# Performance work log

Measured on AMD Instinct MI355X. Metric: run time of the kernel, lower is better.

Reference implementation:

```python
import jax, jax.numpy as jnp
import numpy as np

N_NODES = 100000
N_EDGES = 1600000
IN_FEATS = 128
HIDDEN = 256
NUM_CLASSES = 1


def setup_inputs() -> dict:
    key = jax.random.key(0)
    ks = jax.random.split(key, 6)
    x = jax.random.normal(ks[0], (N_NODES, IN_FEATS), dtype=jnp.float32)
    src = jax.random.randint(ks[1], (N_EDGES,), 0, N_NODES, dtype=jnp.int64 if jax.config.jax_enable_x64 else jnp.int32).astype(jnp.int32)
    dst = jax.random.randint(ks[2], (N_EDGES,), 0, N_NODES, dtype=jnp.int32)
    W1 = jax.random.normal(ks[3], (IN_FEATS, HIDDEN), dtype=jnp.float32) * (1.0 / np.sqrt(IN_FEATS))
    b1 = jnp.zeros((HIDDEN,), dtype=jnp.float32)
    W2 = jax.random.normal(ks[4], (HIDDEN, NUM_CLASSES), dtype=jnp.float32) * (1.0 / np.sqrt(HIDDEN))
    b2 = jnp.zeros((NUM_CLASSES,), dtype=jnp.float32)
    return {"x": x, "src": src, "dst": dst, "W1": W1, "b1": b1, "W2": W2, "b2": b2}


def _graph_conv(x, src, dst, W, b):
    """DGL GraphConv with norm='both': D_out^{-1/2} gather -> scatter-add -> D_in^{-1/2}, then XW+b."""
    n = x.shape[0]
    ones = jnp.ones(src.shape[0], dtype=x.dtype)
    deg_out = jax.ops.segment_sum(ones, src, num_segments=n)
    deg_in = jax.ops.segment_sum(ones, dst, num_segments=n)
    norm_out = jax.lax.rsqrt(jnp.maximum(deg_out, 1.0))  # [N]
    norm_in = jax.lax.rsqrt(jnp.maximum(deg_in, 1.0))    # [N]
    h = x * norm_out[:, None]                 # [N, F]
    msg = h[src]                              # [E, F] gather (memory-bound)
    agg = jax.ops.segment_sum(msg, dst, num_segments=n)  # [N, F] scatter-add
    agg = agg * norm_in[:, None]
    return agg @ W + b


def reference(x, src, dst, W1, b1, W2, b2):
    # layer 0: GraphConv -> relu (dropout p=0.0 -> identity)
    h = jax.nn.relu(_graph_conv(x, src, dst, W1, b1))
    # output layer: GraphConv -> sigmoid
    h = jax.nn.sigmoid(_graph_conv(h, src, dst, W2, b2))
    return h
```

## Files before the change

kernel.cpp:

```cpp
#include <hip/hip_runtime.h>
#include <math.h>

#define NN 100000
#define NE 1600000
#define INF 128
#define HID 256
#define SCAN_BLK 256
#define NSCAN ((NN + SCAN_BLK - 1) / SCAN_BLK)
#define FGRP 8
#define FRNG (NN / FGRP)
#define NC 32
#define CHUNK (NE / NC)

typedef short bf16x8 __attribute__((ext_vector_type(8)));
typedef float f32x4 __attribute__((ext_vector_type(4)));

__device__ __forceinline__ unsigned int f2bf(float f) {
    unsigned int u = __float_as_uint(f);
    u = u + 0x7FFFu + ((u >> 16) & 1u);
    return u >> 16;
}

__launch_bounds__(1024)
__global__ void k_hist(const int* __restrict__ src, const int* __restrict__ dst,
                       int* __restrict__ hist_out, int* __restrict__ hist_in) {
    __shared__ int h[FRNG];
    const int type = blockIdx.x & 1;
    const int g = (blockIdx.x >> 1) & (FGRP - 1);
    const int c = blockIdx.x >> 4;
    const int lo = g * FRNG;
    for (int i = threadIdx.x; i < FRNG; i += 1024) h[i] = 0;
    __syncthreads();
    const int4* a4 = reinterpret_cast<const int4*>((type ? dst : src) + c * CHUNK);
    for (int k = threadIdx.x; k < CHUNK / 4; k += 1024) {
        int4 v = a4[k];
        int i0 = v.x - lo, i1 = v.y - lo, i2 = v.z - lo, i3 = v.w - lo;
        if ((unsigned)i0 < FRNG) atomicAdd(&h[i0], 1);
        if ((unsigned)i1 < FRNG) atomicAdd(&h[i1], 1);
        if ((unsigned)i2 < FRNG) atomicAdd(&h[i2], 1);
        if ((unsigned)i3 < FRNG) atomicAdd(&h[i3], 1);
    }
    __syncthreads();
    int* out = (type ? hist_in : hist_out) + (size_t)c * NN + lo;
    for (int i = threadIdx.x; i < FRNG; i += 1024) out[i] = h[i];
}

__global__ void k_norms2(const int* __restrict__ hist_out, const int* __restrict__ hist_in,
                         float* __restrict__ nrm_out, float* __restrict__ nrm_in,
                         int* __restrict__ deg_in) {
    int v = blockIdx.x * blockDim.x + threadIdx.x;
    if (v < NN) {
        int so = 0, si = 0;
        #pragma unroll
        for (int b = 0; b < NC; ++b) {
            so += hist_out[(size_t)b * NN + v];
            si += hist_in[(size_t)b * NN + v];
        }
        nrm_out[v] = rsqrtf(fmaxf((float)so, 1.0f));
        nrm_in[v]  = rsqrtf(fmaxf((float)si, 1.0f));
        deg_in[v]  = si;
    }
}

__global__ void k_xconv(const float* __restrict__ x, const float* __restrict__ nrm_out,
                        unsigned int* __restrict__ xs) {
    int i = blockIdx.x * blockDim.x + threadIdx.x;
    if (i >= NN * (INF / 2)) return;
    int row = i >> 6;
    float n = nrm_out[row];
    float2 v = *reinterpret_cast<const float2*>(x + (size_t)i * 2);
    xs[i] = f2bf(v.x * n) | (f2bf(v.y * n) << 16);
}

__global__ void k_wfrag(const float* __restrict__ W1, const float* __restrict__ b1,
                        const float* __restrict__ W2, unsigned short* __restrict__ fragW,
                        float2* __restrict__ bw) {
    int idx = blockIdx.x * blockDim.x + threadIdx.x;
    if (idx < 4096) {
        int l = idx & 63, ks = (idx >> 6) & 3, nt = idx >> 8;
        int kbase = ks * 32 + ((l >> 4) << 3);
        int col = nt * 16 + (l & 15);
        bf16x8 r;
        #pragma unroll
        for (int i = 0; i < 8; ++i)
            r[i] = (short)f2bf(W1[(size_t)(kbase + i) * HID + col]);
        *reinterpret_cast<bf16x8*>(fragW + (size_t)idx * 8) = r;
    } else if (idx < 4096 + HID) {
        int n = idx - 4096;
        bw[n] = make_float2(b1[n], W2[n]);
    }
}

__global__ void k_scan1(const int* __restrict__ deg_in, int* __restrict__ partial) {
    __shared__ int sh[SCAN_BLK];
    int i = blockIdx.x * SCAN_BLK + threadIdx.x;
    int v = (i < NN) ? deg_in[i] : 0;
    sh[threadIdx.x] = v;
    __syncthreads();
    for (int off = SCAN_BLK / 2; off > 0; off >>= 1) {
        if (threadIdx.x < off) sh[threadIdx.x] += sh[threadIdx.x + off];
        __syncthreads();
    }
    if (threadIdx.x == 0) partial[blockIdx.x] = sh[0];
}

__global__ void k_scan2(int* __restrict__ partial) {
    int lane = threadIdx.x;
    int carry = 0;
    for (int c = 0; c < NSCAN; c += 64) {
        int idx = c + lane;
        int v = (idx < NSCAN) ? partial[idx] : 0;
        int s = v;
        #pragma unroll
        for (int off = 1; off < 64; off <<= 1) {
            int t = __shfl_up(s, off, 64);
            if (lane >= off) s += t;
        }
        if (idx < NSCAN) partial[idx] = s - v + carry;
        carry += __shfl(s, 63, 64);
    }
}

__global__ void k_scan3(const int* __restrict__ deg_in, const int* __restrict__ partial,
                        int* __restrict__ offsets) {
    __shared__ int sh[SCAN_BLK];
    int i = blockIdx.x * SCAN_BLK + threadIdx.x;
    int v = (i < NN) ? deg_in[i] : 0;
    sh[threadIdx.x] = v;
    __syncthreads();
    for (int off = 1; off < SCAN_BLK; off <<= 1) {
        int t = (threadIdx.x >= off) ? sh[threadIdx.x - off] : 0;
        __syncthreads();
        sh[threadIdx.x] += t;
        __syncthreads();
    }
    int ex = sh[threadIdx.x] - v + partial[blockIdx.x];
    if (i < NN) offsets[i] = ex;
    if (i == 0) offsets[NN] = NE;
}

__global__ void k_cbase(const int* __restrict__ offsets, const int* __restrict__ hist_in,
                        int* __restrict__ cbase) {
    int v = blockIdx.x * blockDim.x + threadIdx.x;
    if (v < NN) {
        int run = offsets[v];
        #pragma unroll
        for (int b = 0; b < NC; ++b) {
            cbase[(size_t)b * NN + v] = run;
            run += hist_in[(size_t)b * NN + v];
        }
    }
}

__launch_bounds__(1024)
__global__ void k_fill2(const int* __restrict__ src, const int* __restrict__ dst,
                        const int* __restrict__ cbase, int* __restrict__ csr_src) {
    __shared__ int cur[FRNG];
    const int g = blockIdx.x & (FGRP - 1);
    const int c = blockIdx.x >> 3;
    const int lo = g * FRNG;
    const int* cb = cbase + (size_t)c * NN + lo;
    for (int i = threadIdx.x; i < FRNG; i += 1024) cur[i] = cb[i];
    __syncthreads();
    const int e0 = c * CHUNK;
    const int4* d4 = reinterpret_cast<const int4*>(dst + e0);
    for (int k = threadIdx.x; k < CHUNK / 4; k += 1024) {
        int4 v = d4[k];
        int e = e0 + k * 4;
        int i0 = v.x - lo, i1 = v.y - lo, i2 = v.z - lo, i3 = v.w - lo;
        if ((unsigned)i0 < FRNG) { int p = atomicAdd(&cur[i0], 1); csr_src[p] = src[e]; }
        if ((unsigned)i1 < FRNG) { int p = atomicAdd(&cur[i1], 1); csr_src[p] = src[e + 1]; }
        if ((unsigned)i2 < FRNG) { int p = atomicAdd(&cur[i2], 1); csr_src[p] = src[e + 2]; }
        if ((unsigned)i3 < FRNG) { int p = atomicAdd(&cur[i3], 1); csr_src[p] = src[e + 3]; }
    }
}

__global__ void k_gather(const unsigned int* __restrict__ xs, const int* __restrict__ offsets,
                         const int* __restrict__ csr_src, const float* __restrict__ nrm_in,
                         unsigned int* __restrict__ aggb) {
    int row = blockIdx.x * 4 + (threadIdx.x >> 6);
    if (row >= NN) return;
    int lane = threadIdx.x & 63;
    int beg = offsets[row], end = offsets[row + 1];
    float a0 = 0.f, a1 = 0.f, b0 = 0.f, b1 = 0.f;
    float c0 = 0.f, c1 = 0.f, d0 = 0.f, d1 = 0.f;
    int j = beg;
    if (j + 4 <= end) {
        int s0 = csr_src[j], s1 = csr_src[j + 1], s2 = csr_src[j + 2], s3 = csr_src[j + 3];
        while (true) {
            unsigned int p0 = xs[(size_t)s0 * 64 + lane];
            unsigned int p1 = xs[(size_t)s1 * 64 + lane];
            unsigned int p2 = xs[(size_t)s2 * 64 + lane];
            unsigned int p3 = xs[(size_t)s3 * 64 + lane];
            j += 4;
            bool more = (j + 4 <= end);
            if (more) {
                s0 = csr_src[j]; s1 = csr_src[j + 1]; s2 = csr_src[j + 2]; s3 = csr_src[j + 3];
            }
            a0 += __uint_as_float(p0 << 16); a1 += __uint_as_float(p0 & 0xFFFF0000u);
            b0 += __uint_as_float(p1 << 16); b1 += __uint_as_float(p1 & 0xFFFF0000u);
            c0 += __uint_as_float(p2 << 16); c1 += __uint_as_float(p2 & 0xFFFF0000u);
            d0 += __uint_as_float(p3 << 16); d1 += __uint_as_float(p3 & 0xFFFF0000u);
            if (!more) break;
        }
    }
    for (; j < end; ++j) {
        unsigned int p0 = xs[(size_t)csr_src[j] * 64 + lane];
        a0 += __uint_as_float(p0 << 16);
        a1 += __uint_as_float(p0 & 0xFFFF0000u);
    }
    float ni = nrm_in[row];
    float lo = ((a0 + b0) + (c0 + d0)) * ni;
    float hi = ((a1 + b1) + (c1 + d1)) * ni;
    aggb[(size_t)row * 64 + lane] = f2bf(lo) | (f2bf(hi) << 16);
}

__launch_bounds__(256)
__global__ void k_gemm(const unsigned short* __restrict__ aggb,
                       const unsigned short* __restrict__ fragW,
                       const float2* __restrict__ bw, const float* __restrict__ nrm_out,
                       float* __restrict__ z) {
    const int l = threadIdx.x & 63;
    const int w = threadIdx.x >> 6;
    const int r0 = blockIdx.x * 64 + w * 16;
    const int n15 = l & 15;
    const int hi = l >> 4;
    const int arow = r0 + n15;

    bf16x8 a[4];
    if (arow < NN) {
        #pragma unroll
        for (int ks = 0; ks < 4; ++ks)
            a[ks] = *reinterpret_cast<const bf16x8*>(aggb + (size_t)arow * INF + ks * 32 + (hi << 3));
    } else {
        #pragma unroll
        for (int ks = 0; ks < 4; ++ks) a[ks] = (bf16x8){0, 0, 0, 0, 0, 0, 0, 0};
    }

    float pacc[4] = {0.f, 0.f, 0.f, 0.f};
    #pragma unroll
    for (int nt = 0; nt < 16; ++nt) {
        f32x4 acc = {0.f, 0.f, 0.f, 0.f};
        #pragma unroll
        for (int ks = 0; ks < 4; ++ks) {
            bf16x8 b = *reinterpret_cast<const bf16x8*>(fragW + (size_t)(((nt * 4 + ks) * 64 + l) << 3));
            acc = __builtin_amdgcn_mfma_f32_16x16x32_bf16(a[ks], b, acc, 0, 0, 0);
        }
        float2 c = bw[nt * 16 + n15];
        #pragma unroll
        for (int g = 0; g < 4; ++g)
            pacc[g] += fmaxf(acc[g] + c.x, 0.f) * c.y;
    }
    #pragma unroll
    for (int off = 1; off < 16; off <<= 1) {
        #pragma unroll
        for (int g = 0; g < 4; ++g) pacc[g] += __shfl_xor(pacc[g], off, 64);
    }
    if (n15 == 0) {
        #pragma unroll
        for (int g = 0; g < 4; ++g) {
            int gr = r0 + (hi << 2) + g;
            if (gr < NN) z[gr] = nrm_out[gr] * pacc[g];
        }
    }
}

__global__ void k_out(const float* __restrict__ z, const int* __restrict__ offsets,
                      const int* __restrict__ csr_src, const float* __restrict__ nrm_in,
                      const float* __restrict__ b2, float* __restrict__ out) {
    int v = blockIdx.x * 16 + (threadIdx.x >> 4);
    if (v >= NN) return;
    int li = threadIdx.x & 15;
    int beg = offsets[v], end = offsets[v + 1];
    float s = 0.f;
    for (int j = beg + li; j < end; j += 16) s += z[csr_src[j]];
    #pragma unroll
    for (int off = 1; off < 16; off <<= 1) s += __shfl_xor(s, off, 64);
    if (li == 0) {
        float val = s * nrm_in[v] + b2[0];
        out[v] = 1.0f / (1.0f + expf(-val));
    }
}

extern "C" void kernel_launch(void* const* d_in, const int* in_sizes, int n_in,
                              void* d_out, int out_size, void* d_ws, size_t ws_size,
                              hipStream_t stream) {
    const float* x   = (const float*)d_in[0];
    const int*   src = (const int*)d_in[1];
    const int*   dst = (const int*)d_in[2];
    const float* W1  = (const float*)d_in[3];
    const float* b1  = (const float*)d_in[4];
    const float* W2  = (const float*)d_in[5];
    const float* b2  = (const float*)d_in[6];
    float* out = (float*)d_out;

    int*   deg_in  = (int*)d_ws;
    int*   offsets = deg_in + NN;
    int*   partial = offsets + NN + 1;
    int*   csr_src = partial + NSCAN;
    float* nrm_out = (float*)(csr_src + NE);
    float* nrm_in  = nrm_out + NN;
    float* z       = nrm_in + NN;
    float2* bw     = (float2*)(z + NN);
    unsigned int* xs   = (unsigned int*)(bw + HID);
    unsigned int* aggb = xs + (size_t)NN * 64;
    unsigned short* fragW = (unsigned short*)(aggb + (size_t)NN * 64);
    int* hist_out = (int*)xs;
    int* hist_in  = hist_out + (size_t)NC * NN;
    int* cbase    = hist_in + (size_t)NC * NN;

    k_wfrag<<<17, 256, 0, stream>>>(W1, b1, W2, fragW, bw);
    k_hist<<<2 * FGRP * NC, 1024, 0, stream>>>(src, dst, hist_out, hist_in);
    k_norms2<<<(NN + 255) / 256, 256, 0, stream>>>(hist_out, hist_in, nrm_out, nrm_in, deg_in);
    k_scan1<<<NSCAN, SCAN_BLK, 0, stream>>>(deg_in, partial);
    k_scan2<<<1, 64, 0, stream>>>(partial);
    k_scan3<<<NSCAN, SCAN_BLK, 0, stream>>>(deg_in, partial, offsets);
    k_cbase<<<(NN + 255) / 256, 256, 0, stream>>>(offsets, hist_in, cbase);
    k_xconv<<<(NN * 64 + 255) / 256, 256, 0, stream>>>(x, nrm_out, xs);
    k_fill2<<<FGRP * NC, 1024, 0, stream>>>(src, dst, cbase, csr_src);
    k_gather<<<NN / 4, 256, 0, stream>>>(xs, offsets, csr_src, nrm_in, aggb);
    k_gemm<<<(NN + 63) / 64, 256, 0, stream>>>((const unsigned short*)aggb, fragW, bw, nrm_out, z);
    k_out<<<(NN + 15) / 16, 256, 0, stream>>>(z, offsets, csr_src, nrm_in, b2, out);
}
```

Baseline: 204.9 us.

## Pack degree histograms into 16-bit counters and fuse scan/cbase kernels

The per-chunk degree histograms now use 16-bit packed counters, two per 32-bit word. This halves shared-memory and global histogram traffic and lets each block cover a quarter of the node range instead of an eighth. The block-sum step of the scan is folded into the norms kernel and the cbase computation into the third scan kernel, which removes two launches and re-reads. cbase moves into the aggb buffer and fill now runs before xconv so that xs can hold the packed histograms; this relies on per-chunk counts staying below 65536.

```diff
diff --git a/kernel.cpp b/kernel.cpp
--- a/kernel.cpp
+++ b/kernel.cpp
@@ -11,6 +11,7 @@
 #define FRNG (NN / FGRP)
 #define NC 32
 #define CHUNK (NE / NC)
+#define HRNG 25000
 
 typedef short bf16x8 __attribute__((ext_vector_type(8)));
 typedef float f32x4 __attribute__((ext_vector_type(4)));
@@ -23,43 +24,52 @@
 
 __launch_bounds__(1024)
 __global__ void k_hist(const int* __restrict__ src, const int* __restrict__ dst,
-                       int* __restrict__ hist_out, int* __restrict__ hist_in) {
-    __shared__ int h[FRNG];
+                       unsigned int* __restrict__ hop, unsigned int* __restrict__ hip) {
+    __shared__ unsigned int h[HRNG / 2];
     const int type = blockIdx.x & 1;
-    const int g = (blockIdx.x >> 1) & (FGRP - 1);
-    const int c = blockIdx.x >> 4;
-    const int lo = g * FRNG;
-    for (int i = threadIdx.x; i < FRNG; i += 1024) h[i] = 0;
+    const int gp = (blockIdx.x >> 1) & 3;
+    const int c = blockIdx.x >> 3;
+    const int lo = gp * HRNG;
+    for (int i = threadIdx.x; i < HRNG / 2; i += 1024) h[i] = 0;
     __syncthreads();
     const int4* a4 = reinterpret_cast<const int4*>((type ? dst : src) + c * CHUNK);
     for (int k = threadIdx.x; k < CHUNK / 4; k += 1024) {
         int4 v = a4[k];
         int i0 = v.x - lo, i1 = v.y - lo, i2 = v.z - lo, i3 = v.w - lo;
-        if ((unsigned)i0 < FRNG) atomicAdd(&h[i0], 1);
-        if ((unsigned)i1 < FRNG) atomicAdd(&h[i1], 1);
-        if ((unsigned)i2 < FRNG) atomicAdd(&h[i2], 1);
-        if ((unsigned)i3 < FRNG) atomicAdd(&h[i3], 1);
-    }
-    __syncthreads();
-    int* out = (type ? hist_in : hist_out) + (size_t)c * NN + lo;
-    for (int i = threadIdx.x; i < FRNG; i += 1024) out[i] = h[i];
-}
-
-__global__ void k_norms2(const int* __restrict__ hist_out, const int* __restrict__ hist_in,
+        if ((unsigned)i0 < HRNG) atomicAdd(&h[i0 >> 1], 1u << ((i0 & 1) << 4));
+        if ((unsigned)i1 < HRNG) atomicAdd(&h[i1 >> 1], 1u << ((i1 & 1) << 4));
+        if ((unsigned)i2 < HRNG) atomicAdd(&h[i2 >> 1], 1u << ((i2 & 1) << 4));
+        if ((unsigned)i3 < HRNG) atomicAdd(&h[i3 >> 1], 1u << ((i3 & 1) << 4));
+    }
+    __syncthreads();
+    unsigned int* o = (type ? hip : hop) + (size_t)c * (NN / 2) + gp * (HRNG / 2);
+    for (int i = threadIdx.x; i < HRNG / 2; i += 1024) o[i] = h[i];
+}
+
+__global__ void k_norms2(const unsigned int* __restrict__ hop, const unsigned int* __restrict__ hip,
                          float* __restrict__ nrm_out, float* __restrict__ nrm_in,
-                         int* __restrict__ deg_in) {
-    int v = blockIdx.x * blockDim.x + threadIdx.x;
+                         int* __restrict__ deg_in, int* __restrict__ partial) {
+    __shared__ int sh[SCAN_BLK];
+    int v = blockIdx.x * SCAN_BLK + threadIdx.x;
+    int so = 0, si = 0;
     if (v < NN) {
-        int so = 0, si = 0;
-        #pragma unroll
-        for (int b = 0; b < NC; ++b) {
-            so += hist_out[(size_t)b * NN + v];
-            si += hist_in[(size_t)b * NN + v];
+        int w = v >> 1, sft = (v & 1) << 4;
+        #pragma unroll
+        for (int c = 0; c < NC; ++c) {
+            so += (hop[(size_t)c * (NN / 2) + w] >> sft) & 0xFFFFu;
+            si += (hip[(size_t)c * (NN / 2) + w] >> sft) & 0xFFFFu;
         }
         nrm_out[v] = rsqrtf(fmaxf((float)so, 1.0f));
         nrm_in[v]  = rsqrtf(fmaxf((float)si, 1.0f));
         deg_in[v]  = si;
     }
+    sh[threadIdx.x] = si;
+    __syncthreads();
+    for (int off = SCAN_BLK / 2; off > 0; off >>= 1) {
+        if (threadIdx.x < off) sh[threadIdx.x] += sh[threadIdx.x + off];
+        __syncthreads();
+    }
+    if (threadIdx.x == 0) partial[blockIdx.x] = sh[0];
 }
 
 __global__ void k_xconv(const float* __restrict__ x, const float* __restrict__ nrm_out,
@@ -91,19 +101,6 @@
     }
 }
 
-__global__ void k_scan1(const int* __restrict__ deg_in, int* __restrict__ partial) {
-    __shared__ int sh[SCAN_BLK];
-    int i = blockIdx.x * SCAN_BLK + threadIdx.x;
-    int v = (i < NN) ? deg_in[i] : 0;
-    sh[threadIdx.x] = v;
-    __syncthreads();
-    for (int off = SCAN_BLK / 2; off > 0; off >>= 1) {
-        if (threadIdx.x < off) sh[threadIdx.x] += sh[threadIdx.x + off];
-        __syncthreads();
-    }
-    if (threadIdx.x == 0) partial[blockIdx.x] = sh[0];
-}
-
 __global__ void k_scan2(int* __restrict__ partial) {
     int lane = threadIdx.x;
     int carry = 0;
@@ -121,8 +118,9 @@
     }
 }
 
-__global__ void k_scan3(const int* __restrict__ deg_in, const int* __restrict__ partial,
-                        int* __restrict__ offsets) {
+__global__ void k_scan3c(const int* __restrict__ deg_in, const int* __restrict__ partial,
+                         int* __restrict__ offsets, const unsigned int* __restrict__ hip,
+                         int* __restrict__ cbase) {
     __shared__ int sh[SCAN_BLK];
     int i = blockIdx.x * SCAN_BLK + threadIdx.x;
     int v = (i < NN) ? deg_in[i] : 0;
@@ -135,21 +133,17 @@
         __syncthreads();
     }
     int ex = sh[threadIdx.x] - v + partial[blockIdx.x];
-    if (i < NN) offsets[i] = ex;
+    if (i < NN) {
+        offsets[i] = ex;
+        int run = ex;
+        int w = i >> 1, sft = (i & 1) << 4;
+        #pragma unroll
+        for (int c = 0; c < NC; ++c) {
+            cbase[(size_t)c * NN + i] = run;
+            run += (hip[(size_t)c * (NN / 2) + w] >> sft) & 0xFFFFu;
+        }
+    }
     if (i == 0) offsets[NN] = NE;
-}
-
-__global__ void k_cbase(const int* __restrict__ offsets, const int* __restrict__ hist_in,
-                        int* __restrict__ cbase) {
-    int v = blockIdx.x * blockDim.x + threadIdx.x;
-    if (v < NN) {
-        int run = offsets[v];
-        #pragma unroll
-        for (int b = 0; b < NC; ++b) {
-            cbase[(size_t)b * NN + v] = run;
-            run += hist_in[(size_t)b * NN + v];
-        }
-    }
 }
 
 __launch_bounds__(1024)
@@ -305,19 +299,17 @@
     unsigned int* xs   = (unsigned int*)(bw + HID);
     unsigned int* aggb = xs + (size_t)NN * 64;
     unsigned short* fragW = (unsigned short*)(aggb + (size_t)NN * 64);
-    int* hist_out = (int*)xs;
-    int* hist_in  = hist_out + (size_t)NC * NN;
-    int* cbase    = hist_in + (size_t)NC * NN;
+    unsigned int* hop = xs;
+    unsigned int* hip = hop + (size_t)NC * (NN / 2);
+    int* cbase = (int*)aggb;
 
     k_wfrag<<<17, 256, 0, stream>>>(W1, b1, W2, fragW, bw);
-    k_hist<<<2 * FGRP * NC, 1024, 0, stream>>>(src, dst, hist_out, hist_in);
-    k_norms2<<<(NN + 255) / 256, 256, 0, stream>>>(hist_out, hist_in, nrm_out, nrm_in, deg_in);
-    k_scan1<<<NSCAN, SCAN_BLK, 0, stream>>>(deg_in, partial);
+    k_hist<<<2 * 4 * NC, 1024, 0, stream>>>(src, dst, hop, hip);
+    k_norms2<<<NSCAN, SCAN_BLK, 0, stream>>>(hop, hip, nrm_out, nrm_in, deg_in, partial);
     k_scan2<<<1, 64, 0, stream>>>(partial);
-    k_scan3<<<NSCAN, SCAN_BLK, 0, stream>>>(deg_in, partial, offsets);
-    k_cbase<<<(NN + 255) / 256, 256, 0, stream>>>(offsets, hist_in, cbase);
+    k_scan3c<<<NSCAN, SCAN_BLK, 0, stream>>>(deg_in, partial, offsets, hip, cbase);
+    k_fill2<<<FGRP * NC, 1024, 0, stream>>>(src, dst, cbase, csr_src);
     k_xconv<<<(NN * 64 + 255) / 256, 256, 0, stream>>>(x, nrm_out, xs);
-    k_fill2<<<FGRP * NC, 1024, 0, stream>>>(src, dst, cbase, csr_src);
     k_gather<<<NN / 4, 256, 0, stream>>>(xs, offsets, csr_src, nrm_in, aggb);
     k_gemm<<<(NN + 63) / 64, 256, 0, stream>>>((const unsigned short*)aggb, fragW, bw, nrm_out, z);
     k_out<<<(NN + 15) / 16, 256, 0, stream>>>(z, offsets, csr_src, nrm_in, b2, out);
```

Result: no change. 206.4 us (+0.7%).
